# Optimization experiments

Measured on AMD Instinct MI355X. Metric: run time of the kernel, lower is better.

## Reference

```python
import jax, jax.numpy as jnp
import numpy as np

B, N, MODEL_D = 2, 1024, 2048
KQ_D, V_D, H, I = 128, 128, 8, 4
ROPE_THETA = 10000.0


def _rope(x, theta):
    # x: [b, n, ..., d]; positions along axis 1, rotation over last dim d.
    d = x.shape[-1]
    n = x.shape[1]
    inv_freq = theta ** (-jnp.arange(0, d, 2, dtype=jnp.float32) / d)  # [d/2]
    ang = jnp.arange(n, dtype=jnp.float32)[:, None] * inv_freq          # [n, d/2]
    bshape = (1, n) + (1,) * (x.ndim - 3) + (d // 2,)
    cos = jnp.cos(ang).reshape(bshape).astype(x.dtype)
    sin = jnp.sin(ang).reshape(bshape).astype(x.dtype)
    x1, x2 = jnp.split(x, 2, axis=-1)
    return jnp.concatenate([x1 * cos - x2 * sin, x1 * sin + x2 * cos], axis=-1)


def setup_inputs() -> dict:
    key = jax.random.key(0)
    kx, kq, kk, kv, ko = jax.random.split(key, 5)
    s_in = 1.0 / np.sqrt(MODEL_D)
    s_out = 1.0 / np.sqrt(H * I * V_D)
    x = jax.random.normal(kx, (B, N, MODEL_D), jnp.float32)
    Wq = jax.random.normal(kq, (MODEL_D, H, I, KQ_D), jnp.float32) * s_in
    Wk = jax.random.normal(kk, (MODEL_D, H, KQ_D), jnp.float32) * s_in
    Wv = jax.random.normal(kv, (MODEL_D, H, V_D), jnp.float32) * s_in
    Wo = jax.random.normal(ko, (H, I, V_D, MODEL_D), jnp.float32) * s_out
    return {"x": x, "Wq": Wq, "Wk": Wk, "Wv": Wv, "Wo": Wo}


def reference(x, Wq, Wk, Wv, Wo):
    # GQA projections (per Ueajsum specs)
    q = jnp.einsum('bnd,dhik->bnhik', x, Wq)   # [B,N,H,I,K]
    k = jnp.einsum('bnd,dhc->bnhc', x, Wk)     # [B,N,H,K]
    v = jnp.einsum('bnd,dhv->bnhv', x, Wv)     # [B,N,H,V]
    # RoPE on q and k
    q = _rope(q, ROPE_THETA)
    k = _rope(k, ROPE_THETA)
    # Causal softmax attention, each kv head serves I query heads
    scale = 1.0 / np.sqrt(KQ_D)
    scores = jnp.einsum('bnhic,bmhc->bhinm', q, k) * scale  # [B,H,I,N,N]
    n = x.shape[1]
    causal = jnp.tril(jnp.ones((n, n), dtype=bool))
    scores = jnp.where(causal, scores, jnp.finfo(scores.dtype).min)
    p = jax.nn.softmax(scores, axis=-1)
    out = jnp.einsum('bhinm,bmhv->bnhiv', p, v)              # [B,N,H,I,V]
    return jnp.einsum('bnhiv,hivd->bnd', out, Wo)            # [B,N,D]
```

## Files before the change

kernel.cpp:

```cpp
#include <hip/hip_runtime.h>
#include <hip/hip_bf16.h>

typedef __bf16 bf16x8 __attribute__((ext_vector_type(8)));
typedef float floatx4 __attribute__((ext_vector_type(4)));

static __device__ __forceinline__ void async_cp16(const __bf16* g, __bf16* l) {
    typedef const __attribute__((address_space(1))) unsigned int gu32;
    typedef __attribute__((address_space(3))) unsigned int lu32;
    __builtin_amdgcn_global_load_lds((gu32*)g, (lu32*)l, 16, 0, 0);
}

__global__ void convert_kernel(const float* __restrict__ src,
                               __bf16* __restrict__ dst, int n8)
{
    int idx = blockIdx.x * blockDim.x + threadIdx.x;
    if (idx >= n8) return;
    const float* p = src + (size_t)idx * 8;
    float4 f0 = *(const float4*)p;
    float4 f1 = *(const float4*)(p + 4);
    union { uint4 u; __bf16 b[8]; } o;
    o.b[0] = (__bf16)f0.x; o.b[1] = (__bf16)f0.y; o.b[2] = (__bf16)f0.z; o.b[3] = (__bf16)f0.w;
    o.b[4] = (__bf16)f1.x; o.b[5] = (__bf16)f1.y; o.b[6] = (__bf16)f1.z; o.b[7] = (__bf16)f1.w;
    *(uint4*)(dst + (size_t)idx * 8) = o.u;
}

__global__ void transpose_cvt_kernel(const float* __restrict__ src,
                                     __bf16* __restrict__ dst, int R, int C)
{
    __shared__ float tile[32][33];
    const int tx = threadIdx.x, ty = threadIdx.y;
    const int c0 = blockIdx.x * 32, r0 = blockIdx.y * 32;
    #pragma unroll
    for (int j = 0; j < 4; ++j)
        tile[ty * 4 + j][tx] = src[(size_t)(r0 + ty * 4 + j) * C + c0 + tx];
    __syncthreads();
    #pragma unroll
    for (int j = 0; j < 4; ++j)
        dst[(size_t)(c0 + ty * 4 + j) * R + r0 + tx] = (__bf16)tile[tx][ty * 4 + j];
}

__global__ void vtrans_kernel(const __bf16* __restrict__ qkv,
                              __bf16* __restrict__ vt)
{
    __shared__ __bf16 tile[32][33];
    const int tx = threadIdx.x, ty = threadIdx.y;
    const int k0 = blockIdx.x * 32, v0 = blockIdx.y * 32;
    const int bh = blockIdx.z;
    const int b = bh >> 3, h = bh & 7;
    #pragma unroll
    for (int j = 0; j < 4; ++j)
        tile[ty * 4 + j][tx] =
            qkv[(size_t)(b * 1024 + k0 + ty * 4 + j) * 6144 + 5120 + h * 128 + v0 + tx];
    __syncthreads();
    #pragma unroll
    for (int j = 0; j < 4; ++j)
        vt[((size_t)bh * 128 + v0 + ty * 4 + j) * 1024 + k0 + tx] = tile[tx][ty * 4 + j];
}

template <typename TC>
__global__ __launch_bounds__(256) void gemm_bt(
    const __bf16* __restrict__ A,
    const __bf16* __restrict__ Bt,
    TC* __restrict__ C,
    int M, int N, int K)
{
    __shared__ __bf16 As[128 * 32];
    __shared__ __bf16 Bs[128 * 32];

    const int tid  = threadIdx.x;
    const int wave = tid >> 6;
    const int lane = tid & 63;
    const int quad = lane >> 4;
    const int l15  = lane & 15;
    const int wr   = wave >> 1, wc = wave & 1;

    const int bm = blockIdx.y * 128;
    const int bn = blockIdx.x * 128;

    floatx4 acc[16];
    #pragma unroll
    for (int i = 0; i < 16; ++i) acc[i] = floatx4{0.f, 0.f, 0.f, 0.f};

    const __bf16* a0 = A  + (size_t)(bm + wave * 32 + (lane >> 2)) * K + (lane & 3) * 8;
    const __bf16* b0 = Bt + (size_t)(bn + wave * 32 + (lane >> 2)) * K + (lane & 3) * 8;
    __bf16* asd0 = As + (wave * 32) * 32;
    __bf16* asd1 = As + (wave * 32 + 16) * 32;
    __bf16* bsd0 = Bs + (wave * 32) * 32;
    __bf16* bsd1 = Bs + (wave * 32 + 16) * 32;

    for (int k0 = 0; k0 < K; k0 += 32) {
        __syncthreads();
        async_cp16(a0 + k0,                  asd0);
        async_cp16(a0 + (size_t)16 * K + k0, asd1);
        async_cp16(b0 + k0,                  bsd0);
        async_cp16(b0 + (size_t)16 * K + k0, bsd1);
        __syncthreads();

        bf16x8 af[4], bf[4];
        #pragma unroll
        for (int t = 0; t < 4; ++t)
            af[t] = *(const bf16x8*)(&As[(wr * 64 + t * 16 + l15) * 32 + quad * 8]);
        #pragma unroll
        for (int u = 0; u < 4; ++u)
            bf[u] = *(const bf16x8*)(&Bs[(wc * 64 + u * 16 + l15) * 32 + quad * 8]);
        #pragma unroll
        for (int t = 0; t < 4; ++t)
            #pragma unroll
            for (int u = 0; u < 4; ++u)
                acc[t * 4 + u] = __builtin_amdgcn_mfma_f32_16x16x32_bf16(
                    af[t], bf[u], acc[t * 4 + u], 0, 0, 0);
    }

    #pragma unroll
    for (int t = 0; t < 4; ++t)
        #pragma unroll
        for (int u = 0; u < 4; ++u)
            #pragma unroll
            for (int r = 0; r < 4; ++r) {
                int row = bm + wr * 64 + t * 16 + quad * 4 + r;
                int col = bn + wc * 64 + u * 16 + l15;
                C[(size_t)row * N + col] = (TC)acc[t * 4 + u][r];
            }
}

template <typename TC>
__global__ __launch_bounds__(256) void gemm_bt64(
    const __bf16* __restrict__ A,
    const __bf16* __restrict__ Bt,
    TC* __restrict__ C,
    int M, int N, int K)
{
    __shared__ __bf16 As[128 * 32];
    __shared__ __bf16 Bs[64 * 32];

    const int tid  = threadIdx.x;
    const int wave = tid >> 6;
    const int lane = tid & 63;
    const int quad = lane >> 4;
    const int l15  = lane & 15;
    const int wr   = wave >> 1, wc = wave & 1;

    const int bm = blockIdx.y * 128;
    const int bn = blockIdx.x * 64;

    floatx4 acc[8];
    #pragma unroll
    for (int i = 0; i < 8; ++i) acc[i] = floatx4{0.f, 0.f, 0.f, 0.f};

    const __bf16* a0 = A  + (size_t)(bm + wave * 32 + (lane >> 2)) * K + (lane & 3) * 8;
    const __bf16* b0 = Bt + (size_t)(bn + wave * 16 + (lane >> 2)) * K + (lane & 3) * 8;
    __bf16* asd0 = As + (wave * 32) * 32;
    __bf16* asd1 = As + (wave * 32 + 16) * 32;
    __bf16* bsd0 = Bs + (wave * 16) * 32;

    for (int k0 = 0; k0 < K; k0 += 32) {
        __syncthreads();
        async_cp16(a0 + k0,                  asd0);
        async_cp16(a0 + (size_t)16 * K + k0, asd1);
        async_cp16(b0 + k0,                  bsd0);
        __syncthreads();

        bf16x8 af[4], bf[2];
        #pragma unroll
        for (int t = 0; t < 4; ++t)
            af[t] = *(const bf16x8*)(&As[(wr * 64 + t * 16 + l15) * 32 + quad * 8]);
        #pragma unroll
        for (int u = 0; u < 2; ++u)
            bf[u] = *(const bf16x8*)(&Bs[(wc * 32 + u * 16 + l15) * 32 + quad * 8]);
        #pragma unroll
        for (int t = 0; t < 4; ++t)
            #pragma unroll
            for (int u = 0; u < 2; ++u)
                acc[t * 2 + u] = __builtin_amdgcn_mfma_f32_16x16x32_bf16(
                    af[t], bf[u], acc[t * 2 + u], 0, 0, 0);
    }

    #pragma unroll
    for (int t = 0; t < 4; ++t)
        #pragma unroll
        for (int u = 0; u < 2; ++u)
            #pragma unroll
            for (int r = 0; r < 4; ++r) {
                int row = bm + wr * 64 + t * 16 + quad * 4 + r;
                int col = bn + wc * 32 + u * 16 + l15;
                C[(size_t)row * N + col] = (TC)acc[t * 2 + u][r];
            }
}

__global__ void rope_kernel(__bf16* __restrict__ qkv, int total)
{
    int idx = blockIdx.x * blockDim.x + threadIdx.x;
    if (idx >= total) return;
    int part = idx & 7;
    int t    = idx >> 3;
    int head = t % 40;
    int row  = t / 40;
    int n    = row & 1023;

    int col0 = (head < 32) ? head * 128 : 4096 + (head - 32) * 128;
    size_t base = (size_t)row * 6144 + col0 + part * 8;

    union { uint4 u; __bf16 b[8]; } x1, x2, o1, o2;
    x1.u = *(const uint4*)(qkv + base);
    x2.u = *(const uint4*)(qkv + base + 64);
    #pragma unroll
    for (int e = 0; e < 8; ++e) {
        int j = part * 8 + e;
        float inv_freq = exp2f(-(float)j * 0.20762050593046015f);
        float ang = (float)n * inv_freq;
        float sv, cv;
        __sincosf(ang, &sv, &cv);
        float a = (float)x1.b[e], b2 = (float)x2.b[e];
        o1.b[e] = (__bf16)(a * cv - b2 * sv);
        o2.b[e] = (__bf16)(a * sv + b2 * cv);
    }
    *(uint4*)(qkv + base)      = o1.u;
    *(uint4*)(qkv + base + 64) = o2.u;
}

__global__ __launch_bounds__(512, 2) void attn_kernel(
    const __bf16* __restrict__ qkv,
    const __bf16* __restrict__ vt,
    __bf16* __restrict__ ao)
{
    const int PS_LD = 72;
    __shared__ __bf16 Ks[64 * 128];
    __shared__ __bf16 Vs[128 * 64];
    __shared__ __bf16 Ps[8][16 * PS_LD];

    const int tid  = threadIdx.x;
    const int wave = tid >> 6;
    const int lane = tid & 63;
    const int quad = lane >> 4;
    const int l15  = lane & 15;
    const int i    = wave >> 1;
    const int rt   = wave & 1;

    const int pair = blockIdx.x;
    const int bh   = blockIdx.y;
    const int b    = bh >> 3, h = bh & 7;
    const __bf16* vtb = vt + (size_t)bh * 128 * 1024;

    const int keyA = wave * 8 + (lane >> 4);
    const int keyB = keyA + 4;
    const int chA  = (lane & 15) ^ (keyA & 15);
    const int chB  = (lane & 15) ^ (keyB & 15);
    const __bf16* gK0 = qkv + (size_t)(b * 1024 + keyA) * 6144 + 4096 + h * 128 + chA * 8;
    const __bf16* gK1 = qkv + (size_t)(b * 1024 + keyB) * 6144 + 4096 + h * 128 + chB * 8;
    __bf16* lK0 = Ks + (wave * 8) * 128;
    __bf16* lK1 = Ks + (wave * 8 + 4) * 128;

    const int vdA = wave * 16 + (lane >> 3);
    const int vdB = vdA + 8;
    const int cvA = (lane & 7) ^ (vdA & 7);
    const int cvB = (lane & 7) ^ (vdB & 7);
    const __bf16* gV0 = vtb + (size_t)vdA * 1024 + cvA * 8;
    const __bf16* gV1 = vtb + (size_t)vdB * 1024 + cvB * 8;
    __bf16* lV0 = Vs + (wave * 16) * 64;
    __bf16* lV1 = Vs + (wave * 16 + 8) * 64;

    bf16x8 onesf;
    #pragma unroll
    for (int j = 0; j < 8; ++j) onesf[j] = (__bf16)1.0f;

    const float C2 = 0.12751898549f;

    #pragma unroll
    for (int ph = 0; ph < 2; ++ph) {
        const int qt    = ph ? (31 - pair) : pair;
        const int qrow0 = qt * 32 + rt * 16;

        const __bf16* qp = qkv + (size_t)(b * 1024 + qrow0 + l15) * 6144 + (h * 4 + i) * 128;
        bf16x8 qf[4];
        #pragma unroll
        for (int c = 0; c < 4; ++c)
            qf[c] = *(const bf16x8*)(qp + c * 32 + quad * 8);

        floatx4 acc[8];
        #pragma unroll
        for (int u = 0; u < 8; ++u) acc[u] = floatx4{0.f, 0.f, 0.f, 0.f};
        floatx4 accl = floatx4{0.f, 0.f, 0.f, 0.f};

        const int ntiles = (qt >> 1) + 1;
        for (int t = 0; t < ntiles; ++t) {
            const int kt = t * 64;
            __syncthreads();
            async_cp16(gK0 + (size_t)kt * 6144, lK0);
            async_cp16(gK1 + (size_t)kt * 6144, lK1);
            async_cp16(gV0 + kt, lV0);
            async_cp16(gV1 + kt, lV1);
            __syncthreads();

            floatx4 s[4];
            #pragma unroll
            for (int ks = 0; ks < 4; ++ks) s[ks] = floatx4{0.f, 0.f, 0.f, 0.f};
            #pragma unroll
            for (int c = 0; c < 4; ++c) {
                #pragma unroll
                for (int ks = 0; ks < 4; ++ks) {
                    bf16x8 kf = *(const bf16x8*)(
                        &Ks[(ks * 16 + l15) * 128 + ((c * 4 + quad) ^ l15) * 8]);
                    s[ks] = __builtin_amdgcn_mfma_f32_16x16x32_bf16(qf[c], kf, s[ks], 0, 0, 0);
                }
            }

            #pragma unroll
            for (int r = 0; r < 4; ++r) {
                int qrow = qrow0 + quad * 4 + r;
                #pragma unroll
                for (int ks = 0; ks < 4; ++ks) {
                    int kc = kt + ks * 16 + l15;
                    float p = (kc <= qrow) ? exp2f(s[ks][r] * C2) : 0.0f;
                    Ps[wave][(quad * 4 + r) * PS_LD + ks * 16 + l15] = (__bf16)p;
                }
            }

            #pragma unroll
            for (int s2 = 0; s2 < 2; ++s2) {
                bf16x8 pa = *(const bf16x8*)(&Ps[wave][l15 * PS_LD + s2 * 32 + quad * 8]);
                accl = __builtin_amdgcn_mfma_f32_16x16x32_bf16(pa, onesf, accl, 0, 0, 0);
                #pragma unroll
                for (int u = 0; u < 8; ++u) {
                    bf16x8 vf = *(const bf16x8*)(
                        &Vs[(u * 16 + l15) * 64 + (((s2 * 4 + quad) ^ (l15 & 7))) * 8]);
                    acc[u] = __builtin_amdgcn_mfma_f32_16x16x32_bf16(pa, vf, acc[u], 0, 0, 0);
                }
            }
        }

        #pragma unroll
        for (int r = 0; r < 4; ++r) {
            float inv = 1.0f / accl[r];
            int row = qrow0 + quad * 4 + r;
            __bf16* op = ao + (size_t)(b * 1024 + row) * 4096 + (h * 4 + i) * 128;
            #pragma unroll
            for (int u = 0; u < 8; ++u)
                op[u * 16 + l15] = (__bf16)(acc[u][r] * inv);
        }
    }
}

extern "C" void kernel_launch(void* const* d_in, const int* in_sizes, int n_in,
                              void* d_out, int out_size, void* d_ws, size_t ws_size,
                              hipStream_t stream)
{
    const float* x  = (const float*)d_in[0];
    const float* Wq = (const float*)d_in[1];
    const float* Wk = (const float*)d_in[2];
    const float* Wv = (const float*)d_in[3];
    const float* Wo = (const float*)d_in[4];
    float* out = (float*)d_out;

    const size_t MB = 1024 * 1024;
    char* ws = (char*)d_ws;
    __bf16* qkv = (__bf16*)(ws);
    __bf16* vtb = (__bf16*)(ws + 24 * MB);
    __bf16* xb  = (__bf16*)(ws + 28 * MB);
    __bf16* Wt  = (__bf16*)(ws + 36 * MB);
    __bf16* ao  = (__bf16*)(ws + 28 * MB);
    __bf16* WoT = (__bf16*)(ws + 44 * MB);

    dim3 t32x8(32, 8);

    convert_kernel<<<2048, 256, 0, stream>>>(x, xb, 4194304 / 8);
    transpose_cvt_kernel<<<dim3(128, 64), t32x8, 0, stream>>>(Wq, Wt, 2048, 4096);
    transpose_cvt_kernel<<<dim3(32, 64),  t32x8, 0, stream>>>(Wk, Wt + (size_t)4096 * 2048, 2048, 1024);
    transpose_cvt_kernel<<<dim3(32, 64),  t32x8, 0, stream>>>(Wv, Wt + (size_t)5120 * 2048, 2048, 1024);
    gemm_bt<__bf16><<<dim3(48, 16), 256, 0, stream>>>(xb, Wt, qkv, 2048, 6144, 2048);
    transpose_cvt_kernel<<<dim3(64, 128), t32x8, 0, stream>>>(Wo, WoT, 4096, 2048);
    rope_kernel<<<(2048 * 40 * 8 + 255) / 256, 256, 0, stream>>>(qkv, 2048 * 40 * 8);
    vtrans_kernel<<<dim3(32, 4, 16), t32x8, 0, stream>>>(qkv, vtb);
    attn_kernel<<<dim3(16, 16), 512, 0, stream>>>(qkv, vtb, ao);
    gemm_bt64<float><<<dim3(32, 16), 256, 0, stream>>>(ao, WoT, out, 2048, 2048, 4096);
}
```

Measured before the change: 337.7 us.

## Fuse prep and rope/vtrans kernels, split-K output GEMM with reduce

Merges x conversion and Wq/Wk/Wv transposes into one launch, and rope with V transpose into another, to cut launch count. The output projection switches from a 128x64-tile GEMM to a 128x128-tile GEMM split across K in two halves, writing bf16 partials that a separate reduce kernel sums into fp32 output. This aims for better tile reuse and occupancy, but adds a partial-buffer round trip and rounds partials to bf16.

Result: faster. 323.5 us (-4.2%).

```diff
diff --git a/kernel.cpp b/kernel.cpp
--- a/kernel.cpp
+++ b/kernel.cpp
@@ -10,18 +10,39 @@
     __builtin_amdgcn_global_load_lds((gu32*)g, (lu32*)l, 16, 0, 0);
 }
 
-__global__ void convert_kernel(const float* __restrict__ src,
-                               __bf16* __restrict__ dst, int n8)
-{
-    int idx = blockIdx.x * blockDim.x + threadIdx.x;
-    if (idx >= n8) return;
-    const float* p = src + (size_t)idx * 8;
-    float4 f0 = *(const float4*)p;
-    float4 f1 = *(const float4*)(p + 4);
-    union { uint4 u; __bf16 b[8]; } o;
-    o.b[0] = (__bf16)f0.x; o.b[1] = (__bf16)f0.y; o.b[2] = (__bf16)f0.z; o.b[3] = (__bf16)f0.w;
-    o.b[4] = (__bf16)f1.x; o.b[5] = (__bf16)f1.y; o.b[6] = (__bf16)f1.z; o.b[7] = (__bf16)f1.w;
-    *(uint4*)(dst + (size_t)idx * 8) = o.u;
+__global__ __launch_bounds__(256) void prep_kernel(
+    const float* __restrict__ x,  __bf16* __restrict__ xb,
+    const float* __restrict__ Wq, const float* __restrict__ Wk,
+    const float* __restrict__ Wv, __bf16* __restrict__ Wt)
+{
+    __shared__ float tile[32][33];
+    const int bk  = blockIdx.x;
+    const int tid = threadIdx.x;
+    const int tx  = tid & 31, ty = tid >> 5;
+
+    if (bk < 12288) {
+        const float* src; __bf16* dst; int R = 2048, C; int bxx, byy;
+        if (bk < 8192)        { src = Wq; dst = Wt;                          C = 4096; bxx = bk & 127;           byy = bk >> 7; }
+        else if (bk < 10240)  { src = Wk; dst = Wt + (size_t)4096 * 2048;    C = 1024; bxx = (bk - 8192) & 31;   byy = (bk - 8192) >> 5; }
+        else                  { src = Wv; dst = Wt + (size_t)5120 * 2048;    C = 1024; bxx = (bk - 10240) & 31;  byy = (bk - 10240) >> 5; }
+        const int c0 = bxx * 32, r0 = byy * 32;
+        #pragma unroll
+        for (int j = 0; j < 4; ++j)
+            tile[ty * 4 + j][tx] = src[(size_t)(r0 + ty * 4 + j) * C + c0 + tx];
+        __syncthreads();
+        #pragma unroll
+        for (int j = 0; j < 4; ++j)
+            dst[(size_t)(c0 + ty * 4 + j) * R + r0 + tx] = (__bf16)tile[tx][ty * 4 + j];
+    } else {
+        int idx = (bk - 12288) * 256 + tid;
+        const float* p = x + (size_t)idx * 8;
+        float4 f0 = *(const float4*)p;
+        float4 f1 = *(const float4*)(p + 4);
+        union { uint4 u; __bf16 b[8]; } o;
+        o.b[0] = (__bf16)f0.x; o.b[1] = (__bf16)f0.y; o.b[2] = (__bf16)f0.z; o.b[3] = (__bf16)f0.w;
+        o.b[4] = (__bf16)f1.x; o.b[5] = (__bf16)f1.y; o.b[6] = (__bf16)f1.z; o.b[7] = (__bf16)f1.w;
+        *(uint4*)(xb + (size_t)idx * 8) = o.u;
+    }
 }
 
 __global__ void transpose_cvt_kernel(const float* __restrict__ src,
@@ -39,22 +60,55 @@
         dst[(size_t)(c0 + ty * 4 + j) * R + r0 + tx] = (__bf16)tile[tx][ty * 4 + j];
 }
 
-__global__ void vtrans_kernel(const __bf16* __restrict__ qkv,
-                              __bf16* __restrict__ vt)
+__global__ __launch_bounds__(256) void rope_vtrans_kernel(
+    __bf16* __restrict__ qkv, __bf16* __restrict__ vt)
 {
     __shared__ __bf16 tile[32][33];
-    const int tx = threadIdx.x, ty = threadIdx.y;
-    const int k0 = blockIdx.x * 32, v0 = blockIdx.y * 32;
-    const int bh = blockIdx.z;
-    const int b = bh >> 3, h = bh & 7;
-    #pragma unroll
-    for (int j = 0; j < 4; ++j)
-        tile[ty * 4 + j][tx] =
-            qkv[(size_t)(b * 1024 + k0 + ty * 4 + j) * 6144 + 5120 + h * 128 + v0 + tx];
-    __syncthreads();
-    #pragma unroll
-    for (int j = 0; j < 4; ++j)
-        vt[((size_t)bh * 128 + v0 + ty * 4 + j) * 1024 + k0 + tx] = tile[tx][ty * 4 + j];
+    const int bk  = blockIdx.x;
+    const int tid = threadIdx.x;
+
+    if (bk < 2560) {
+        int idx  = bk * 256 + tid;
+        int part = idx & 7;
+        int t    = idx >> 3;
+        int head = t % 40;
+        int row  = t / 40;
+        int n    = row & 1023;
+        int col0 = (head < 32) ? head * 128 : 4096 + (head - 32) * 128;
+        size_t base = (size_t)row * 6144 + col0 + part * 8;
+
+        union { uint4 u; __bf16 b[8]; } x1, x2, o1, o2;
+        x1.u = *(const uint4*)(qkv + base);
+        x2.u = *(const uint4*)(qkv + base + 64);
+        #pragma unroll
+        for (int e = 0; e < 8; ++e) {
+            int j = part * 8 + e;
+            float inv_freq = exp2f(-(float)j * 0.20762050593046015f);
+            float ang = (float)n * inv_freq;
+            float sv, cv;
+            __sincosf(ang, &sv, &cv);
+            float a = (float)x1.b[e], b2 = (float)x2.b[e];
+            o1.b[e] = (__bf16)(a * cv - b2 * sv);
+            o2.b[e] = (__bf16)(a * sv + b2 * cv);
+        }
+        *(uint4*)(qkv + base)      = o1.u;
+        *(uint4*)(qkv + base + 64) = o2.u;
+    } else {
+        int idx = bk - 2560;
+        const int tx = tid & 31, ty = tid >> 5;
+        const int k0 = (idx & 31) * 32;
+        const int v0 = ((idx >> 5) & 3) * 32;
+        const int bh = idx >> 7;
+        const int b = bh >> 3, h = bh & 7;
+        #pragma unroll
+        for (int j = 0; j < 4; ++j)
+            tile[ty * 4 + j][tx] =
+                qkv[(size_t)(b * 1024 + k0 + ty * 4 + j) * 6144 + 5120 + h * 128 + v0 + tx];
+        __syncthreads();
+        #pragma unroll
+        for (int j = 0; j < 4; ++j)
+            vt[((size_t)bh * 128 + v0 + ty * 4 + j) * 1024 + k0 + tx] = tile[tx][ty * 4 + j];
+    }
 }
 
 template <typename TC>
@@ -62,7 +116,7 @@
     const __bf16* __restrict__ A,
     const __bf16* __restrict__ Bt,
     TC* __restrict__ C,
-    int M, int N, int K)
+    int M, int N, int Kc, int lda, int ldb, int ldc)
 {
     __shared__ __bf16 As[128 * 32];
     __shared__ __bf16 Bs[128 * 32];
@@ -76,24 +130,29 @@
 
     const int bm = blockIdx.y * 128;
     const int bn = blockIdx.x * 128;
+    const int z  = blockIdx.z;
+
+    A  += (size_t)z * Kc;
+    Bt += (size_t)z * Kc;
+    C  += (size_t)z * M * ldc;
 
     floatx4 acc[16];
     #pragma unroll
     for (int i = 0; i < 16; ++i) acc[i] = floatx4{0.f, 0.f, 0.f, 0.f};
 
-    const __bf16* a0 = A  + (size_t)(bm + wave * 32 + (lane >> 2)) * K + (lane & 3) * 8;
-    const __bf16* b0 = Bt + (size_t)(bn + wave * 32 + (lane >> 2)) * K + (lane & 3) * 8;
+    const __bf16* a0 = A  + (size_t)(bm + wave * 32 + (lane >> 2)) * lda + (lane & 3) * 8;
+    const __bf16* b0 = Bt + (size_t)(bn + wave * 32 + (lane >> 2)) * ldb + (lane & 3) * 8;
     __bf16* asd0 = As + (wave * 32) * 32;
     __bf16* asd1 = As + (wave * 32 + 16) * 32;
     __bf16* bsd0 = Bs + (wave * 32) * 32;
     __bf16* bsd1 = Bs + (wave * 32 + 16) * 32;
 
-    for (int k0 = 0; k0 < K; k0 += 32) {
+    for (int k0 = 0; k0 < Kc; k0 += 32) {
         __syncthreads();
-        async_cp16(a0 + k0,                  asd0);
-        async_cp16(a0 + (size_t)16 * K + k0, asd1);
-        async_cp16(b0 + k0,                  bsd0);
-        async_cp16(b0 + (size_t)16 * K + k0, bsd1);
+        async_cp16(a0 + k0,                    asd0);
+        async_cp16(a0 + (size_t)16 * lda + k0, asd1);
+        async_cp16(b0 + k0,                    bsd0);
+        async_cp16(b0 + (size_t)16 * ldb + k0, bsd1);
         __syncthreads();
 
         bf16x8 af[4], bf[4];
@@ -119,103 +178,29 @@
             for (int r = 0; r < 4; ++r) {
                 int row = bm + wr * 64 + t * 16 + quad * 4 + r;
                 int col = bn + wc * 64 + u * 16 + l15;
-                C[(size_t)row * N + col] = (TC)acc[t * 4 + u][r];
+                C[(size_t)row * ldc + col] = (TC)acc[t * 4 + u][r];
             }
 }
 
-template <typename TC>
-__global__ __launch_bounds__(256) void gemm_bt64(
-    const __bf16* __restrict__ A,
-    const __bf16* __restrict__ Bt,
-    TC* __restrict__ C,
-    int M, int N, int K)
-{
-    __shared__ __bf16 As[128 * 32];
-    __shared__ __bf16 Bs[64 * 32];
-
-    const int tid  = threadIdx.x;
-    const int wave = tid >> 6;
-    const int lane = tid & 63;
-    const int quad = lane >> 4;
-    const int l15  = lane & 15;
-    const int wr   = wave >> 1, wc = wave & 1;
-
-    const int bm = blockIdx.y * 128;
-    const int bn = blockIdx.x * 64;
-
-    floatx4 acc[8];
-    #pragma unroll
-    for (int i = 0; i < 8; ++i) acc[i] = floatx4{0.f, 0.f, 0.f, 0.f};
-
-    const __bf16* a0 = A  + (size_t)(bm + wave * 32 + (lane >> 2)) * K + (lane & 3) * 8;
-    const __bf16* b0 = Bt + (size_t)(bn + wave * 16 + (lane >> 2)) * K + (lane & 3) * 8;
-    __bf16* asd0 = As + (wave * 32) * 32;
-    __bf16* asd1 = As + (wave * 32 + 16) * 32;
-    __bf16* bsd0 = Bs + (wave * 16) * 32;
-
-    for (int k0 = 0; k0 < K; k0 += 32) {
-        __syncthreads();
-        async_cp16(a0 + k0,                  asd0);
-        async_cp16(a0 + (size_t)16 * K + k0, asd1);
-        async_cp16(b0 + k0,                  bsd0);
-        __syncthreads();
-
-        bf16x8 af[4], bf[2];
-        #pragma unroll
-        for (int t = 0; t < 4; ++t)
-            af[t] = *(const bf16x8*)(&As[(wr * 64 + t * 16 + l15) * 32 + quad * 8]);
-        #pragma unroll
-        for (int u = 0; u < 2; ++u)
-            bf[u] = *(const bf16x8*)(&Bs[(wc * 32 + u * 16 + l15) * 32 + quad * 8]);
-        #pragma unroll
-        for (int t = 0; t < 4; ++t)
-            #pragma unroll
-            for (int u = 0; u < 2; ++u)
-                acc[t * 2 + u] = __builtin_amdgcn_mfma_f32_16x16x32_bf16(
-                    af[t], bf[u], acc[t * 2 + u], 0, 0, 0);
-    }
-
-    #pragma unroll
-    for (int t = 0; t < 4; ++t)
-        #pragma unroll
-        for (int u = 0; u < 2; ++u)
-            #pragma unroll
-            for (int r = 0; r < 4; ++r) {
-                int row = bm + wr * 64 + t * 16 + quad * 4 + r;
-                int col = bn + wc * 32 + u * 16 + l15;
-                C[(size_t)row * N + col] = (TC)acc[t * 2 + u][r];
-            }
-}
-
-__global__ void rope_kernel(__bf16* __restrict__ qkv, int total)
-{
-    int idx = blockIdx.x * blockDim.x + threadIdx.x;
-    if (idx >= total) return;
-    int part = idx & 7;
-    int t    = idx >> 3;
-    int head = t % 40;
-    int row  = t / 40;
-    int n    = row & 1023;
-
-    int col0 = (head < 32) ? head * 128 : 4096 + (head - 32) * 128;
-    size_t base = (size_t)row * 6144 + col0 + part * 8;
-
-    union { uint4 u; __bf16 b[8]; } x1, x2, o1, o2;
-    x1.u = *(const uint4*)(qkv + base);
-    x2.u = *(const uint4*)(qkv + base + 64);
-    #pragma unroll
-    for (int e = 0; e < 8; ++e) {
-        int j = part * 8 + e;
-        float inv_freq = exp2f(-(float)j * 0.20762050593046015f);
-        float ang = (float)n * inv_freq;
-        float sv, cv;
-        __sincosf(ang, &sv, &cv);
-        float a = (float)x1.b[e], b2 = (float)x2.b[e];
-        o1.b[e] = (__bf16)(a * cv - b2 * sv);
-        o2.b[e] = (__bf16)(a * sv + b2 * cv);
-    }
-    *(uint4*)(qkv + base)      = o1.u;
-    *(uint4*)(qkv + base + 64) = o2.u;
+__global__ __launch_bounds__(256) void reduce_kernel(
+    const __bf16* __restrict__ part, float* __restrict__ out)
+{
+    int idx = blockIdx.x * 256 + threadIdx.x;
+    const size_t STRIDE = (size_t)2048 * 2048;
+    union { uint4 u; __bf16 b[8]; } p0, p1;
+    p0.u = *(const uint4*)(part + (size_t)idx * 8);
+    p1.u = *(const uint4*)(part + STRIDE + (size_t)idx * 8);
+    float4 o0, o1;
+    o0.x = (float)p0.b[0] + (float)p1.b[0];
+    o0.y = (float)p0.b[1] + (float)p1.b[1];
+    o0.z = (float)p0.b[2] + (float)p1.b[2];
+    o0.w = (float)p0.b[3] + (float)p1.b[3];
+    o1.x = (float)p0.b[4] + (float)p1.b[4];
+    o1.y = (float)p0.b[5] + (float)p1.b[5];
+    o1.z = (float)p0.b[6] + (float)p1.b[6];
+    o1.w = (float)p0.b[7] + (float)p1.b[7];
+    *(float4*)(out + (size_t)idx * 8)     = o0;
+    *(float4*)(out + (size_t)idx * 8 + 4) = o1;
 }
 
 __global__ __launch_bounds__(512, 2) void attn_kernel(
@@ -353,23 +338,19 @@
 
     const size_t MB = 1024 * 1024;
     char* ws = (char*)d_ws;
-    __bf16* qkv = (__bf16*)(ws);
-    __bf16* vtb = (__bf16*)(ws + 24 * MB);
-    __bf16* xb  = (__bf16*)(ws + 28 * MB);
-    __bf16* Wt  = (__bf16*)(ws + 36 * MB);
-    __bf16* ao  = (__bf16*)(ws + 28 * MB);
-    __bf16* WoT = (__bf16*)(ws + 44 * MB);
-
-    dim3 t32x8(32, 8);
-
-    convert_kernel<<<2048, 256, 0, stream>>>(x, xb, 4194304 / 8);
-    transpose_cvt_kernel<<<dim3(128, 64), t32x8, 0, stream>>>(Wq, Wt, 2048, 4096);
-    transpose_cvt_kernel<<<dim3(32, 64),  t32x8, 0, stream>>>(Wk, Wt + (size_t)4096 * 2048, 2048, 1024);
-    transpose_cvt_kernel<<<dim3(32, 64),  t32x8, 0, stream>>>(Wv, Wt + (size_t)5120 * 2048, 2048, 1024);
-    gemm_bt<__bf16><<<dim3(48, 16), 256, 0, stream>>>(xb, Wt, qkv, 2048, 6144, 2048);
-    transpose_cvt_kernel<<<dim3(64, 128), t32x8, 0, stream>>>(Wo, WoT, 4096, 2048);
-    rope_kernel<<<(2048 * 40 * 8 + 255) / 256, 256, 0, stream>>>(qkv, 2048 * 40 * 8);
-    vtrans_kernel<<<dim3(32, 4, 16), t32x8, 0, stream>>>(qkv, vtb);
+    __bf16* qkv  = (__bf16*)(ws);
+    __bf16* vtb  = (__bf16*)(ws + 24 * MB);
+    __bf16* xb   = (__bf16*)(ws + 28 * MB);
+    __bf16* Wt   = (__bf16*)(ws + 36 * MB);
+    __bf16* ao   = (__bf16*)(ws + 28 * MB);
+    __bf16* WoT  = (__bf16*)(ws + 44 * MB);
+    __bf16* part = (__bf16*)(ws);
+
+    prep_kernel<<<14336, 256, 0, stream>>>(x, xb, Wq, Wk, Wv, Wt);
+    gemm_bt<__bf16><<<dim3(48, 16), 256, 0, stream>>>(xb, Wt, qkv, 2048, 6144, 2048, 2048, 2048, 6144);
+    transpose_cvt_kernel<<<dim3(64, 128), dim3(32, 8), 0, stream>>>(Wo, WoT, 4096, 2048);
+    rope_vtrans_kernel<<<4608, 256, 0, stream>>>(qkv, vtb);
     attn_kernel<<<dim3(16, 16), 512, 0, stream>>>(qkv, vtb, ao);
-    gemm_bt64<float><<<dim3(32, 16), 256, 0, stream>>>(ao, WoT, out, 2048, 2048, 4096);
-}
+    gemm_bt<__bf16><<<dim3(16, 16, 2), 256, 0, stream>>>(ao, WoT, part, 2048, 2048, 2048, 4096, 4096, 2048);
+    reduce_kernel<<<2048, 256, 0, stream>>>(part, out);
+}
```
